# Optimization experiments

Measured on AMD Instinct MI355X. Metric: run time of the kernel, lower is better.

The kernel has to match this reference:

```python
import jax, jax.numpy as jnp
import numpy as np


def setup_inputs() -> dict:
    key = jax.random.key(0)
    out = jax.random.normal(key, (8388608, 8), dtype=jnp.float32)
    return {"out": out, "num_per_group": 8}


def reference(out, num_per_group):
    # view(-1, num_per_group)
    x = out.reshape(-1, num_per_group)
    # torch: argsort(-out) then take index num_per_group//2 and gather its value.
    # The gathered value equals the element of rank num_per_group//2 in descending
    # order, i.e. ascending-sorted position (num_per_group - 1 - num_per_group//2).
    half = num_per_group // 2
    midv = jnp.sort(x, axis=1)[:, num_per_group - 1 - half][:, None]  # [R, 1]
    mask = (x > midv).astype(x.dtype)                                  # [R, n]
    # nn.Softmax() on a 2D tensor defaults to dim=1
    return jax.nn.softmax(x, axis=1) * mask
```

## Files before the change

### kernel.cpp

```cpp
#include <hip/hip_runtime.h>


typedef float f32x4 __attribute__((ext_vector_type(4)));

#define CMPSWAP(i, j)                     \
    {                                     \
        float lo = fminf(x[i], x[j]);     \
        float hi = fmaxf(x[i], x[j]);     \
        x[i] = lo;                        \
        x[j] = hi;                        \
    }

__global__ __launch_bounds__(256) void HNet3_topk_softmax_kernel(
    const f32x4* __restrict__ in, f32x4* __restrict__ out, int nrows)
{
    int row = blockIdx.x * blockDim.x + threadIdx.x;
    if (row >= nrows) return;

    f32x4 a = __builtin_nontemporal_load(in + 2 * row);
    f32x4 b = __builtin_nontemporal_load(in + 2 * row + 1);

    float v[8] = {a[0], a[1], a[2], a[3], b[0], b[1], b[2], b[3]};
    float x[8];
#pragma unroll
    for (int i = 0; i < 8; ++i) x[i] = v[i];

    CMPSWAP(0, 1) CMPSWAP(2, 3) CMPSWAP(4, 5) CMPSWAP(6, 7)
    CMPSWAP(0, 2) CMPSWAP(1, 3) CMPSWAP(4, 6) CMPSWAP(5, 7)
    CMPSWAP(1, 2) CMPSWAP(5, 6) CMPSWAP(0, 4) CMPSWAP(3, 7)
    CMPSWAP(1, 5) CMPSWAP(2, 6)
    CMPSWAP(1, 4) CMPSWAP(3, 6)
    CMPSWAP(2, 4) CMPSWAP(3, 5)
    CMPSWAP(3, 4)

    float midv = x[3];
    float m    = x[7];

    float e[8];
    float s = 0.f;
#pragma unroll
    for (int i = 0; i < 8; ++i) {
        e[i] = __expf(v[i] - m);
        s += e[i];
    }
    float inv = __builtin_amdgcn_rcpf(s);

    f32x4 oa, ob;
    oa[0] = (v[0] > midv) ? e[0] * inv : 0.f;
    oa[1] = (v[1] > midv) ? e[1] * inv : 0.f;
    oa[2] = (v[2] > midv) ? e[2] * inv : 0.f;
    oa[3] = (v[3] > midv) ? e[3] * inv : 0.f;
    ob[0] = (v[4] > midv) ? e[4] * inv : 0.f;
    ob[1] = (v[5] > midv) ? e[5] * inv : 0.f;
    ob[2] = (v[6] > midv) ? e[6] * inv : 0.f;
    ob[3] = (v[7] > midv) ? e[7] * inv : 0.f;

    __builtin_nontemporal_store(oa, out + 2 * row);
    __builtin_nontemporal_store(ob, out + 2 * row + 1);
}

extern "C" void kernel_launch(void* const* d_in, const int* in_sizes, int n_in,
                              void* d_out, int out_size, void* d_ws, size_t ws_size,
                              hipStream_t stream) {
    const f32x4* in = (const f32x4*)d_in[0];
    f32x4* out      = (f32x4*)d_out;

    int nrows   = in_sizes[0] / 8;
    int threads = 256;
    int blocks  = (nrows + threads - 1) / threads;

    HNet3_topk_softmax_kernel<<<blocks, threads, 0, stream>>>(in, out, nrows);
}
```

Before: 424.2 us.

## Use grid-stride persistent loop with next-row register prefetch

Replaces the one-row-per-thread launch with a fixed 2048-block grid-stride loop. Each thread issues the loads for its next row before computing and storing the current one, so memory latency overlaps with the sort and softmax work. This cuts block launch overhead but lowers the number of independent waves in flight, and it adds register pressure from the prefetched values.

After: 440.9 us. 3.9% more time.

```diff
diff --git a/kernel.cpp b/kernel.cpp
--- a/kernel.cpp
+++ b/kernel.cpp
@@ -3,23 +3,17 @@
 
 typedef float f32x4 __attribute__((ext_vector_type(4)));
 
-#define CMPSWAP(i, j)                     \
-    {                                     \
-        float lo = fminf(x[i], x[j]);     \
-        float hi = fmaxf(x[i], x[j]);     \
-        x[i] = lo;                        \
-        x[j] = hi;                        \
+#define CMPSWAP(i, j)                      \
+    {                                      \
+        float lo_ = fminf(x[i], x[j]);     \
+        float hi_ = fmaxf(x[i], x[j]);     \
+        x[i] = lo_;                        \
+        x[j] = hi_;                        \
     }
 
-__global__ __launch_bounds__(256) void HNet3_topk_softmax_kernel(
-    const f32x4* __restrict__ in, f32x4* __restrict__ out, int nrows)
+__device__ __forceinline__ void process_row(const f32x4& a, const f32x4& b,
+                                            f32x4& oa, f32x4& ob)
 {
-    int row = blockIdx.x * blockDim.x + threadIdx.x;
-    if (row >= nrows) return;
-
-    f32x4 a = __builtin_nontemporal_load(in + 2 * row);
-    f32x4 b = __builtin_nontemporal_load(in + 2 * row + 1);
-
     float v[8] = {a[0], a[1], a[2], a[3], b[0], b[1], b[2], b[3]};
     float x[8];
 #pragma unroll
@@ -45,7 +39,6 @@
     }
     float inv = __builtin_amdgcn_rcpf(s);
 
-    f32x4 oa, ob;
     oa[0] = (v[0] > midv) ? e[0] * inv : 0.f;
     oa[1] = (v[1] > midv) ? e[1] * inv : 0.f;
     oa[2] = (v[2] > midv) ? e[2] * inv : 0.f;
@@ -54,9 +47,38 @@
     ob[1] = (v[5] > midv) ? e[5] * inv : 0.f;
     ob[2] = (v[6] > midv) ? e[6] * inv : 0.f;
     ob[3] = (v[7] > midv) ? e[7] * inv : 0.f;
+}
 
-    __builtin_nontemporal_store(oa, out + 2 * row);
-    __builtin_nontemporal_store(ob, out + 2 * row + 1);
+__global__ __launch_bounds__(256) void HNet3_topk_softmax_kernel(
+    const f32x4* __restrict__ in, f32x4* __restrict__ out, int nrows)
+{
+    const int stride = gridDim.x * blockDim.x;
+    int row = blockIdx.x * blockDim.x + threadIdx.x;
+    if (row >= nrows) return;
+
+    f32x4 a = __builtin_nontemporal_load(in + 2 * row);
+    f32x4 b = __builtin_nontemporal_load(in + 2 * row + 1);
+
+    while (true) {
+        const int next = row + stride;
+
+        f32x4 an, bn;
+        const bool more = (next < nrows);
+        if (more) {
+            an = __builtin_nontemporal_load(in + 2 * next);
+            bn = __builtin_nontemporal_load(in + 2 * next + 1);
+        }
+
+        f32x4 oa, ob;
+        process_row(a, b, oa, ob);
+        __builtin_nontemporal_store(oa, out + 2 * row);
+        __builtin_nontemporal_store(ob, out + 2 * row + 1);
+
+        if (!more) break;
+        row = next;
+        a = an;
+        b = bn;
+    }
 }
 
 extern "C" void kernel_launch(void* const* d_in, const int* in_sizes, int n_in,
@@ -67,7 +89,10 @@
 
     int nrows   = in_sizes[0] / 8;
     int threads = 256;
-    int blocks  = (nrows + threads - 1) / threads;
+
+    int blocks  = 2048;
+    int max_needed = (nrows + threads - 1) / threads;
+    if (blocks > max_needed) blocks = max_needed;
 
     HNet3_topk_softmax_kernel<<<blocks, threads, 0, stream>>>(in, out, nrows);
 }
```
